# Optimization experiments

Measured on AMD Instinct MI355X. Metric: run time of the kernel, lower is better.

## Reference

```python
import jax, jax.numpy as jnp
import numpy as np

B, D, H, W, C = 2, 6, 64, 64, 192
NH = 8                      # num heads
HD = C // NH                # head dim
E, K, HID = 8, 2, 384       # experts, top_k, d_hidden
WS = (2, 8, 8)              # window size (Wd, Wh, Ww)
SS = (1, 4, 4)              # shift size
N = WS[0] * WS[1] * WS[2]   # 128 tokens per window
NW = (D // WS[0]) * (H // WS[1]) * (W // WS[2])  # 192 windows per sample
SCALE = HD ** -0.5


def _rel_pos_index():
    coords = np.stack(np.meshgrid(np.arange(WS[0]), np.arange(WS[1]), np.arange(WS[2]), indexing='ij'))
    coords = coords.reshape(3, -1)
    rel = (coords[:, :, None] - coords[:, None, :]).transpose(1, 2, 0).astype(np.int64)
    rel[..., 0] += WS[0] - 1
    rel[..., 1] += WS[1] - 1
    rel[..., 2] += WS[2] - 1
    rel[..., 0] *= (2 * WS[1] - 1) * (2 * WS[2] - 1)
    rel[..., 1] *= (2 * WS[2] - 1)
    return rel.sum(-1)  # (N, N)


def _sine_pos_encoding():
    # VRT get_sine_position_encoding(window_size[1:], dim//2, normalize=True)
    h, w, nf = WS[1], WS[2], C // 2
    scale = 2 * np.pi
    y = np.cumsum(np.ones((1, h, w)), 1)
    x = np.cumsum(np.ones((1, h, w)), 2)
    y = y / (y[:, -1:, :] + 1e-6) * scale
    x = x / (x[:, :, -1:] + 1e-6) * scale
    dim_t = 10000.0 ** (2 * (np.arange(nf) // 2) / nf)
    px = x[..., None] / dim_t
    py = y[..., None] / dim_t
    px = np.stack([np.sin(px[..., 0::2]), np.cos(px[..., 1::2])], -1).reshape(1, h, w, -1)
    py = np.stack([np.sin(py[..., 0::2]), np.cos(py[..., 1::2])], -1).reshape(1, h, w, -1)
    return np.concatenate([py, px], -1).reshape(1, h * w, C).astype(np.float32)


def _compute_mask():
    # VRT compute_mask for cyclic shift
    img = np.zeros((1, D, H, W, 1))
    cnt = 0
    for d in (slice(0, -WS[0]), slice(-WS[0], -SS[0]), slice(-SS[0], None)):
        for h in (slice(0, -WS[1]), slice(-WS[1], -SS[1]), slice(-SS[1], None)):
            for w in (slice(0, -WS[2]), slice(-WS[2], -SS[2]), slice(-SS[2], None)):
                img[:, d, h, w, :] = cnt
                cnt += 1
    mw = img.reshape(1, D // WS[0], WS[0], H // WS[1], WS[1], W // WS[2], WS[2], 1)
    mw = mw.transpose(0, 1, 3, 5, 2, 4, 6, 7).reshape(-1, N)
    am = mw[:, None, :] - mw[:, :, None]
    return np.where(am != 0, -100.0, 0.0).astype(np.float32)  # (NW, N, N)


RP_INDEX = jnp.asarray(_rel_pos_index())
POS_BIAS = jnp.asarray(_sine_pos_encoding())  # (1, Wh*Ww, C)


def layernorm(x, w, b):
    mu = x.mean(-1, keepdims=True)
    var = ((x - mu) ** 2).mean(-1, keepdims=True)
    return (x - mu) * jax.lax.rsqrt(var + 1e-5) * w + b


def window_partition(x):
    x = x.reshape(B, D // WS[0], WS[0], H // WS[1], WS[1], W // WS[2], WS[2], C)
    return x.transpose(0, 1, 3, 5, 2, 4, 6, 7).reshape(-1, N, C)


def window_reverse(wx):
    x = wx.reshape(B, D // WS[0], H // WS[1], W // WS[2], WS[0], WS[1], WS[2], C)
    return x.transpose(0, 1, 4, 2, 5, 3, 6, 7).reshape(B, D, H, W, C)


def _attn(q, k, v, mask, bias):
    # q,k,v: (B_, NH, n, HD); mask: (NW, N, N) or None; bias: (NH, n, n) or None
    n = q.shape[2]
    a = jnp.einsum('bhnd,bhmd->bhnm', q * SCALE, k)
    if bias is not None:
        a = a + bias[None]
    if mask is not None:
        a = a.reshape(-1, NW, NH, n, n) + mask[None, :, None, :n, :n]
        a = a.reshape(-1, NH, n, n)
    a = jax.nn.softmax(a, -1)
    o = jnp.einsum('bhnm,bhmd->bhnd', a, v)
    return o.transpose(0, 2, 1, 3).reshape(o.shape[0], n, NH * HD)


def reference(x, mask_matrix, n1_w, n1_b, qkv_self_w, qkv_self_b, qkv_mut_w, qkv_mut_b,
              rpb_table, proj_w, proj_b, n2_w, n2_b, gate_w, gate_b, W1, b1, W2, b2):
    # ---- part 1: shifted 3D window attention (self + mutual) ----
    xn = layernorm(x, n1_w, n1_b)
    xs = jnp.roll(xn, shift=(-SS[0], -SS[1], -SS[2]), axis=(1, 2, 3))
    xw = window_partition(xs)  # (B_, N, C)
    B_ = xw.shape[0]

    def qkv_split(t):
        t = t.reshape(B_, -1, 3, NH, HD).transpose(2, 0, 3, 1, 4)
        return t[0], t[1], t[2]

    # self attention with relative position bias
    q, k, v = qkv_split(xw @ qkv_self_w + qkv_self_b)
    bias = rpb_table[RP_INDEX.reshape(-1)].reshape(N, N, NH).transpose(2, 0, 1)
    x_self = _attn(q, k, v, mask_matrix, bias)

    # mutual attention between the two frames of each window
    xm = xw + jnp.tile(POS_BIAS, (1, 2, 1))
    q, k, v = qkv_split(xm @ qkv_mut_w + qkv_mut_b)
    half = N // 2
    q1, q2 = q[:, :, :half], q[:, :, half:]
    k1, k2 = k[:, :, :half], k[:, :, half:]
    v1, v2 = v[:, :, :half], v[:, :, half:]
    x1 = _attn(q2, k1, v1, mask_matrix, None)
    x2 = _attn(q1, k2, v2, mask_matrix, None)
    x_out = jnp.concatenate([jnp.concatenate([x1, x2], 1), x_self], 2)  # (B_, N, 2C)

    attn_out = x_out @ proj_w + proj_b  # (B_, N, C)
    xr = window_reverse(attn_out)
    xr = jnp.roll(xr, shift=SS, axis=(1, 2, 3))
    x = x + xr

    # ---- part 2: MoE FFN (top-2 gate, per-expert 2-layer MLP, weighted combine) ----
    xn = layernorm(x, n2_w, n2_b).reshape(-1, C)  # (T, C)
    logits = xn @ gate_w + gate_b  # (T, E)
    top_val, top_idx = jax.lax.top_k(logits, K)
    scores = jax.nn.softmax(top_val, -1)  # (T, K)
    cw = (jax.nn.one_hot(top_idx, E, dtype=xn.dtype) * scores[..., None]).sum(1)  # (T, E)

    def body(acc, p):
        w1, bb1, w2, bb2, cwe = p
        hdd = jax.nn.gelu(xn @ w1 + bb1, approximate=False)
        return acc + cwe[:, None] * (hdd @ w2 + bb2), None

    moe_out, _ = jax.lax.scan(body, jnp.zeros_like(xn), (W1, b1, W2, b2, cw.T))
    return x + moe_out.reshape(B, D, H, W, C)


def setup_inputs() -> dict:
    key = jax.random.key(0)
    ks = jax.random.split(key, 8)
    s = 0.02
    tbl = (2 * WS[0] - 1) * (2 * WS[1] - 1) * (2 * WS[2] - 1)
    return dict(
        x=jax.random.normal(ks[0], (B, D, H, W, C), jnp.float32),
        mask_matrix=jnp.asarray(_compute_mask()),
        n1_w=jnp.ones((C,), jnp.float32), n1_b=jnp.zeros((C,), jnp.float32),
        qkv_self_w=jax.random.normal(ks[1], (C, 3 * C), jnp.float32) * s,
        qkv_self_b=jnp.zeros((3 * C,), jnp.float32),
        qkv_mut_w=jax.random.normal(ks[2], (C, 3 * C), jnp.float32) * s,
        qkv_mut_b=jnp.zeros((3 * C,), jnp.float32),
        rpb_table=jax.random.normal(ks[3], (tbl, NH), jnp.float32) * s,
        proj_w=jax.random.normal(ks[4], (2 * C, C), jnp.float32) * s,
        proj_b=jnp.zeros((C,), jnp.float32),
        n2_w=jnp.ones((C,), jnp.float32), n2_b=jnp.zeros((C,), jnp.float32),
        gate_w=jax.random.normal(ks[5], (C, E), jnp.float32) * s,
        gate_b=jnp.zeros((E,), jnp.float32),
        W1=jax.random.normal(ks[6], (E, C, HID), jnp.float32) * s,
        b1=jnp.zeros((E, HID), jnp.float32),
        W2=jax.random.normal(ks[7], (E, HID, C), jnp.float32) * s,
        b2=jnp.zeros((E, C), jnp.float32),
    )
```

## Files before the change

kernel.cpp:

```cpp
#include <hip/hip_runtime.h>
#include <hip/hip_bf16.h>

#define NW_ 192
#define NWIN 384
#define NTOK 128
#define CC 192
#define NHD 8
#define HD 24
#define QKVC 576
#define NROWS 49152
#define HIDN 384
#define SCALE_Q 0.20412414523193154f

typedef __hip_bfloat16 bf16;
typedef __attribute__((ext_vector_type(8))) short s16x8;
typedef __attribute__((ext_vector_type(4))) float f32x4;

__device__ __forceinline__ float waveRedSum(float v) {
    v += __shfl_xor(v, 32);
    v += __shfl_xor(v, 16);
    v += __shfl_xor(v, 8);
    v += __shfl_xor(v, 4);
    v += __shfl_xor(v, 2);
    v += __shfl_xor(v, 1);
    return v;
}

__device__ __forceinline__ size_t row_to_x(int r) {
    int wb = r >> 7;
    int n = r & 127;
    int b = wb / NW_;
    int rem = wb % NW_;
    int wd = rem >> 6;
    int wh = (rem >> 3) & 7;
    int ww = rem & 7;
    int id = n >> 6;
    int ih = (n >> 3) & 7;
    int iw = n & 7;
    int d = (wd * 2 + id + 1) % 6;
    int h = (wh * 8 + ih + 4) & 63;
    int w = (ww * 8 + iw + 4) & 63;
    return ((size_t)((b * 6 + d) * 64 + h) * 64 + w) * CC;
}

__device__ __forceinline__ void split_store(float v, bf16* hi, bf16* lo) {
    bf16 h = __float2bfloat16(v);
    *hi = h;
    *lo = __float2bfloat16(v - __bfloat162float(h));
}

__global__ void zero_counts(int* counts) {
    if (threadIdx.x < 8) counts[threadIdx.x] = 0;
}

__global__ __launch_bounds__(256) void transpose_w(
    const float* __restrict__ in, bf16* __restrict__ out_hi,
    bf16* __restrict__ out_lo, int K, int N) {
    size_t total = (size_t)K * N;
    in += (size_t)blockIdx.z * total;
    out_hi += (size_t)blockIdx.z * total;
    int t = blockIdx.x * 256 + threadIdx.x;
    if (t >= (int)total) return;
    int n = t / K, k = t % K;
    float v = in[(size_t)k * N + n];
    bf16 h = __float2bfloat16(v);
    out_hi[t] = h;
    if (out_lo) {
        out_lo += (size_t)blockIdx.z * total;
        out_lo[t] = __float2bfloat16(v - __bfloat162float(h));
    }
}

__global__ __launch_bounds__(256) void build_rpbx(
    const float* __restrict__ rpb, float* __restrict__ rpbx) {
    int idx = blockIdx.x * 256 + threadIdx.x;
    int q = idx >> 7, k = idx & 127;
    int dn = q >> 6, hn = (q >> 3) & 7, wn = q & 7;
    int dm = k >> 6, hm = (k >> 3) & 7, wm = k & 7;
    int ridx = (dn - dm + 1) * 225 + (hn - hm + 7) * 15 + (wn - wm + 7);
#pragma unroll
    for (int h = 0; h < 8; ++h)
        rpbx[h * 16384 + idx] = rpb[ridx * 8 + h];
}

__global__ __launch_bounds__(256) void ln1_partition(
    const float* __restrict__ x, const float* __restrict__ n1w,
    const float* __restrict__ n1b, bf16* __restrict__ xw_hi,
    bf16* __restrict__ xw_lo) {
    int r = blockIdx.x * 4 + (threadIdx.x >> 6);
    int t = threadIdx.x & 63;
    const float* src = x + row_to_x(r);
    float v0 = src[t], v1 = src[t + 64], v2 = src[t + 128];
    float mu = waveRedSum(v0 + v1 + v2) * (1.0f / 192.0f);
    float d0 = v0 - mu, d1 = v1 - mu, d2 = v2 - mu;
    float var = waveRedSum(d0 * d0 + d1 * d1 + d2 * d2) * (1.0f / 192.0f);
    float rstd = rsqrtf(var + 1e-5f);
    size_t b = (size_t)r * CC;
    split_store(d0 * rstd * n1w[t]       + n1b[t],       xw_hi + b + t,       xw_lo + b + t);
    split_store(d1 * rstd * n1w[t + 64]  + n1b[t + 64],  xw_hi + b + t + 64,  xw_lo + b + t + 64);
    split_store(d2 * rstd * n1w[t + 128] + n1b[t + 128], xw_hi + b + t + 128, xw_lo + b + t + 128);
}

__global__ __launch_bounds__(256) void add_posbias(
    bf16* __restrict__ hi, bf16* __restrict__ lo) {
    int idx = blockIdx.x * 256 + threadIdx.x;
    if (idx >= NROWS * CC) return;
    int c = idx % CC;
    int r = idx / CC;
    int n = r & 127;
    int tkn = n & 63;
    int h = tkn >> 3, w = tkn & 7;
    const float twopi_over = 6.283185307179586f / (8.0f + 1e-6f);
    float coord = (c < 96) ? (h + 1) * twopi_over : (w + 1) * twopi_over;
    int cc = (c < 96) ? c : c - 96;
    int j = cc >> 1;
    float v = coord * __expf(-0.1918820910968785f * (float)j);
    float pe = (cc & 1) ? __cosf(v) : __sinf(v);
    float val = __bfloat162float(hi[idx]) + __bfloat162float(lo[idx]) + pe;
    split_store(val, hi + idx, lo + idx);
}

template <int EPI, int GSHIFT, bool GATHER, bool SPLIT>
__global__ __launch_bounds__(256) void mgemm(
    const bf16* __restrict__ A, const bf16* __restrict__ Alo, int ldA,
    const bf16* __restrict__ Wt, const bf16* __restrict__ Wtlo, int wStrideE,
    const float* __restrict__ bias, int biasStrideE,
    float* __restrict__ Cf, bf16* __restrict__ Cb,
    int M, int K, int N,
    const int* __restrict__ counts, const int* __restrict__ lists,
    const float* __restrict__ wts, const float* __restrict__ xres) {
    int e = blockIdx.z;
    int Mq = counts ? counts[e] : M;
    int bm = blockIdx.x * 128;
    if (bm >= Mq) return;
    int bn = blockIdx.y * 64;
    const int lbase = e * NROWS;
    __shared__ __align__(16) bf16 As[128][72];
    __shared__ __align__(16) bf16 Bs[64][72];
    __shared__ __align__(16) bf16 Asl[(SPLIT ? 128 : 1)][72];
    __shared__ __align__(16) bf16 Bsl[(SPLIT ? 64 : 1)][72];
    int t = threadIdx.x;
    int arow = t >> 1, acol = (t & 1) * 32;
    int brow = t >> 2, bcol = (t & 3) * 16;
    size_t aoff;
    if (GATHER) {
        int p = bm + arow;
        int a = lists[lbase + (p < Mq ? p : 0)];
        aoff = (size_t)(a >> GSHIFT) * (size_t)ldA + acol;
    } else {
        aoff = (size_t)(bm + arow) * (size_t)ldA + acol;
    }
    size_t boff = (size_t)e * wStrideE + (size_t)(bn + brow) * K + bcol;
    int wv = t >> 6, l = t & 63;
    int wvm = wv >> 1, wvn = wv & 1;
    int fr = l & 15, fg = l >> 4;
    f32x4 acc[4][2];
#pragma unroll
    for (int mf = 0; mf < 4; ++mf)
#pragma unroll
        for (int nf = 0; nf < 2; ++nf) acc[mf][nf] = (f32x4){0.f, 0.f, 0.f, 0.f};
    for (int k0 = 0; k0 < K; k0 += 64) {
        __syncthreads();
#pragma unroll
        for (int u = 0; u < 4; ++u)
            *(int4*)&As[arow][acol + u * 8] = *(const int4*)(A + aoff + k0 + u * 8);
        *(int4*)&Bs[brow][bcol]     = *(const int4*)(Wt + boff + k0);
        *(int4*)&Bs[brow][bcol + 8] = *(const int4*)(Wt + boff + k0 + 8);
        if (SPLIT) {
#pragma unroll
            for (int u = 0; u < 4; ++u)
                *(int4*)&Asl[arow][acol + u * 8] = *(const int4*)(Alo + aoff + k0 + u * 8);
            *(int4*)&Bsl[brow][bcol]     = *(const int4*)(Wtlo + boff + k0);
            *(int4*)&Bsl[brow][bcol + 8] = *(const int4*)(Wtlo + boff + k0 + 8);
        }
        __syncthreads();
#pragma unroll
        for (int ks = 0; ks < 2; ++ks) {
            s16x8 ah[4], al[4], bh[2], bl[2];
#pragma unroll
            for (int mf = 0; mf < 4; ++mf) {
                ah[mf] = *(const s16x8*)&As[wvm * 64 + mf * 16 + fr][ks * 32 + fg * 8];
                if (SPLIT) al[mf] = *(const s16x8*)&Asl[wvm * 64 + mf * 16 + fr][ks * 32 + fg * 8];
            }
#pragma unroll
            for (int nf = 0; nf < 2; ++nf) {
                bh[nf] = *(const s16x8*)&Bs[wvn * 32 + nf * 16 + fr][ks * 32 + fg * 8];
                if (SPLIT) bl[nf] = *(const s16x8*)&Bsl[wvn * 32 + nf * 16 + fr][ks * 32 + fg * 8];
            }
#pragma unroll
            for (int mf = 0; mf < 4; ++mf)
#pragma unroll
                for (int nf = 0; nf < 2; ++nf) {
                    acc[mf][nf] = __builtin_amdgcn_mfma_f32_16x16x32_bf16(ah[mf], bh[nf], acc[mf][nf], 0, 0, 0);
                    if (SPLIT) {
                        acc[mf][nf] = __builtin_amdgcn_mfma_f32_16x16x32_bf16(ah[mf], bl[nf], acc[mf][nf], 0, 0, 0);
                        acc[mf][nf] = __builtin_amdgcn_mfma_f32_16x16x32_bf16(al[mf], bh[nf], acc[mf][nf], 0, 0, 0);
                    }
                }
        }
    }
#pragma unroll
    for (int mf = 0; mf < 4; ++mf) {
        int row0 = bm + wvm * 64 + mf * 16 + fg * 4;
        if (EPI == 0) {
#pragma unroll
            for (int nf = 0; nf < 2; ++nf) {
                int c = bn + wvn * 32 + nf * 16 + fr;
                float bv = bias[c];
#pragma unroll
                for (int i = 0; i < 4; ++i)
                    Cf[(size_t)(row0 + i) * N + c] = acc[mf][nf][i] + bv;
            }
        } else if (EPI == 1) {
            size_t sr[4];
#pragma unroll
            for (int i = 0; i < 4; ++i) sr[i] = row_to_x(row0 + i);
#pragma unroll
            for (int nf = 0; nf < 2; ++nf) {
                int c = bn + wvn * 32 + nf * 16 + fr;
                float bv = bias[c];
#pragma unroll
                for (int i = 0; i < 4; ++i)
                    Cf[sr[i] + c] = xres[sr[i] + c] + acc[mf][nf][i] + bv;
            }
        } else if (EPI == 2) {
            const float* bp = bias + (size_t)e * biasStrideE;
#pragma unroll
            for (int i = 0; i < 4; ++i) {
                int p = row0 + i;
                if (p < Mq) {
                    int a = lists[lbase + p];
#pragma unroll
                    for (int nf = 0; nf < 2; ++nf) {
                        int c = bn + wvn * 32 + nf * 16 + fr;
                        float v = acc[mf][nf][i] + bp[c];
                        float g = 0.5f * v * (1.0f + erff(v * 0.7071067811865476f));
                        Cb[(size_t)a * HIDN + c] = __float2bfloat16(g);
                    }
                }
            }
        } else if (EPI == 3) {
            const float* bp = bias + (size_t)e * biasStrideE;
#pragma unroll
            for (int i = 0; i < 4; ++i) {
                int p = row0 + i;
                if (p < Mq) {
                    int a = lists[lbase + p];
                    int r = a >> 1;
                    float w = wts[lbase + p];
#pragma unroll
                    for (int nf = 0; nf < 2; ++nf) {
                        int c = bn + wvn * 32 + nf * 16 + fr;
                        atomicAdd(&Cf[(size_t)r * CC + c], w * (acc[mf][nf][i] + bp[c]));
                    }
                }
            }
        } else {
            const size_t S0 = (size_t)NROWS * 192;
            const size_t S1 = (size_t)NROWS * 24;
#pragma unroll
            for (int nf = 0; nf < 2; ++nf) {
                int c = bn + wvn * 32 + nf * 16 + fr;
                int which = c / 192;
                int rem = c - which * 192;
                int hh = rem / 24;
                int d = rem - hh * 24;
                float bv = bias[c];
                bf16* hb = Cb + (size_t)(2 * which) * S0 + (size_t)hh * S1;
                bf16* lb = Cb + (size_t)(2 * which + 1) * S0 + (size_t)hh * S1;
#pragma unroll
                for (int i = 0; i < 4; ++i) {
                    float v = acc[mf][nf][i] + bv;
                    if (which == 0) v *= SCALE_Q;
                    size_t o = (size_t)(row0 + i) * 24 + d;
                    split_store(v, hb + o, lb + o);
                }
            }
        }
    }
}

template <bool SELF>
__global__ __launch_bounds__(256) void attn_mfma(
    const bf16* __restrict__ qkvp, const float* __restrict__ mask,
    const float* __restrict__ rpbx, bf16* __restrict__ cat_hi,
    bf16* __restrict__ cat_lo) {
    constexpr int NT = SELF ? 128 : 64;
    constexpr int KT = NT / 16;
    constexpr int CPW = NT / 64;
    constexpr int KS = NT / 32;
    const size_t S0 = (size_t)NROWS * 192;
    const size_t S1 = (size_t)NROWS * 24;

    int wb = blockIdx.x, hh = blockIdx.y;
    int hf = SELF ? 0 : blockIdx.z;
    int qbase = wb * NTOK + (SELF ? 0 : (hf ? 0 : 64));
    int kvbase = wb * NTOK + (SELF ? 0 : (hf ? 64 : 0));
    int t = threadIdx.x;
    int wv = t >> 6, l = t & 63, fr = l & 15, fg = l >> 4;

    __shared__ __align__(16) ushort Vth[32][144];
    __shared__ __align__(16) ushort Vtl[32][144];
    __shared__ float linv_s[NT];

    {
        constexpr int PPT = 256 / NT;
        constexpr int DP = 24 / PPT;
        int tok = t % NT;
        int part = t / NT;
        const ushort* vh = (const ushort*)(qkvp + 4 * S0) + hh * S1 +
                           (size_t)(kvbase + tok) * 24 + part * DP;
        const ushort* vl = (const ushort*)(qkvp + 5 * S0) + hh * S1 +
                           (size_t)(kvbase + tok) * 24 + part * DP;
#pragma unroll
        for (int u = 0; u < DP; ++u) {
            Vth[part * DP + u][tok] = vh[u];
            Vtl[part * DP + u][tok] = vl[u];
        }
    }

    s16x8 zf = {0, 0, 0, 0, 0, 0, 0, 0};
    f32x4 st[KT][CPW];
#pragma unroll
    for (int kt = 0; kt < KT; ++kt)
#pragma unroll
        for (int c = 0; c < CPW; ++c) st[kt][c] = (f32x4){0.f, 0.f, 0.f, 0.f};

    s16x8 qfh[CPW], qfl[CPW];
#pragma unroll
    for (int c = 0; c < CPW; ++c) {
        int qt = wv * CPW + c;
        const bf16* qrow = qkvp + hh * S1 + (size_t)(qbase + qt * 16 + fr) * 24 + fg * 8;
        qfh[c] = (fg < 3) ? *(const s16x8*)qrow : zf;
        qfl[c] = (fg < 3) ? *(const s16x8*)(qrow + S0) : zf;
    }
#pragma unroll
    for (int kt = 0; kt < KT; ++kt) {
        const bf16* krow = qkvp + 2 * S0 + hh * S1 + (size_t)(kvbase + kt * 16 + fr) * 24 + fg * 8;
        s16x8 kh = (fg < 3) ? *(const s16x8*)krow : zf;
        s16x8 kl = (fg < 3) ? *(const s16x8*)(krow + S0) : zf;
#pragma unroll
        for (int c = 0; c < CPW; ++c) {
            st[kt][c] = __builtin_amdgcn_mfma_f32_16x16x32_bf16(kh, qfh[c], st[kt][c], 0, 0, 0);
            st[kt][c] = __builtin_amdgcn_mfma_f32_16x16x32_bf16(kh, qfl[c], st[kt][c], 0, 0, 0);
            st[kt][c] = __builtin_amdgcn_mfma_f32_16x16x32_bf16(kl, qfh[c], st[kt][c], 0, 0, 0);
        }
    }

    uint phq[KT][CPW][2], plq[KT][CPW][2];
#pragma unroll
    for (int c = 0; c < CPW; ++c) {
        int q = (wv * CPW + c) * 16 + fr;
        const float* mrow = mask + ((size_t)(wb % NW_) * NTOK + q) * NTOK;
        const float* brow = rpbx + ((size_t)hh * NTOK + q) * NTOK;
        float mx = -1e30f;
#pragma unroll
        for (int kt = 0; kt < KT; ++kt) {
            int k0 = kt * 16 + fg * 4;
            float4 mk = *(const float4*)(mrow + k0);
            if (SELF) {
                float4 bs = *(const float4*)(brow + k0);
                mk.x += bs.x; mk.y += bs.y; mk.z += bs.z; mk.w += bs.w;
            }
            st[kt][c][0] += mk.x; st[kt][c][1] += mk.y;
            st[kt][c][2] += mk.z; st[kt][c][3] += mk.w;
#pragma unroll
            for (int i = 0; i < 4; ++i) mx = fmaxf(mx, st[kt][c][i]);
        }
        mx = fmaxf(mx, __shfl_xor(mx, 16));
        mx = fmaxf(mx, __shfl_xor(mx, 32));
        float ls = 0.f;
#pragma unroll
        for (int kt = 0; kt < KT; ++kt)
#pragma unroll
            for (int i = 0; i < 4; ++i) {
                float pv = __expf(st[kt][c][i] - mx);
                st[kt][c][i] = pv;
                ls += pv;
            }
        ls += __shfl_xor(ls, 16);
        ls += __shfl_xor(ls, 32);
        if (fg == 0) linv_s[q] = 1.0f / ls;
#pragma unroll
        for (int kt = 0; kt < KT; ++kt) {
            ushort hb[4], lb[4];
#pragma unroll
            for (int i = 0; i < 4; ++i) {
                float pv = st[kt][c][i];
                bf16 ph = __float2bfloat16(pv);
                hb[i] = *(ushort*)&ph;
                bf16 pl = __float2bfloat16(pv - __bfloat162float(ph));
                lb[i] = *(ushort*)&pl;
            }
            phq[kt][c][0] = (uint)hb[0] | ((uint)hb[1] << 16);
            phq[kt][c][1] = (uint)hb[2] | ((uint)hb[3] << 16);
            plq[kt][c][0] = (uint)lb[0] | ((uint)lb[1] << 16);
            plq[kt][c][1] = (uint)lb[2] | ((uint)lb[3] << 16);
        }
    }
    __syncthreads();

    f32x4 oacc[CPW][2];
#pragma unroll
    for (int rt = 0; rt < CPW; ++rt)
#pragma unroll
        for (int ct = 0; ct < 2; ++ct) oacc[rt][ct] = (f32x4){0.f, 0.f, 0.f, 0.f};

    int sA = fr + 32 * (fg & 1);
    int sB = sA + 16;
    bool tsel = fg >= 2;
#pragma unroll
    for (int ks = 0; ks < KS; ++ks) {
        s16x8 bh[2], bl[2];
#pragma unroll
        for (int ct = 0; ct < 2; ++ct) {
            bh[ct] = *(const s16x8*)&Vth[ct * 16 + fr][ks * 32 + fg * 8];
            bl[ct] = *(const s16x8*)&Vtl[ct * 16 + fr][ks * 32 + fg * 8];
        }
#pragma unroll
        for (int rt = 0; rt < CPW; ++rt) {
            union { uint u[4]; s16x8 v; } ah, al;
            uint x0, x1;
            x0 = __shfl(phq[2 * ks][rt][0], sA); x1 = __shfl(phq[2 * ks + 1][rt][0], sA);
            ah.u[0] = tsel ? x1 : x0;
            x0 = __shfl(phq[2 * ks][rt][1], sA); x1 = __shfl(phq[2 * ks + 1][rt][1], sA);
            ah.u[1] = tsel ? x1 : x0;
            x0 = __shfl(phq[2 * ks][rt][0], sB); x1 = __shfl(phq[2 * ks + 1][rt][0], sB);
            ah.u[2] = tsel ? x1 : x0;
            x0 = __shfl(phq[2 * ks][rt][1], sB); x1 = __shfl(phq[2 * ks + 1][rt][1], sB);
            ah.u[3] = tsel ? x1 : x0;
            x0 = __shfl(plq[2 * ks][rt][0], sA); x1 = __shfl(plq[2 * ks + 1][rt][0], sA);
            al.u[0] = tsel ? x1 : x0;
            x0 = __shfl(plq[2 * ks][rt][1], sA); x1 = __shfl(plq[2 * ks + 1][rt][1], sA);
            al.u[1] = tsel ? x1 : x0;
            x0 = __shfl(plq[2 * ks][rt][0], sB); x1 = __shfl(plq[2 * ks + 1][rt][0], sB);
            al.u[2] = tsel ? x1 : x0;
            x0 = __shfl(plq[2 * ks][rt][1], sB); x1 = __shfl(plq[2 * ks + 1][rt][1], sB);
            al.u[3] = tsel ? x1 : x0;
#pragma unroll
            for (int ct = 0; ct < 2; ++ct) {
                oacc[rt][ct] = __builtin_amdgcn_mfma_f32_16x16x32_bf16(ah.v, bh[ct], oacc[rt][ct], 0, 0, 0);
                oacc[rt][ct] = __builtin_amdgcn_mfma_f32_16x16x32_bf16(ah.v, bl[ct], oacc[rt][ct], 0, 0, 0);
                oacc[rt][ct] = __builtin_amdgcn_mfma_f32_16x16x32_bf16(al.v, bh[ct], oacc[rt][ct], 0, 0, 0);
            }
        }
    }

#pragma unroll
    for (int rt = 0; rt < CPW; ++rt)
#pragma unroll
        for (int ct = 0; ct < 2; ++ct) {
            int d = ct * 16 + fr;
            if (d < 24) {
#pragma unroll
                for (int i = 0; i < 4; ++i) {
                    int q = (wv * CPW + rt) * 16 + fg * 4 + i;
                    float val = oacc[rt][ct][i] * linv_s[q];
                    int otok = SELF ? q : (hf ? 64 + q : q);
                    size_t ob = (size_t)(wb * NTOK + otok) * 384 + (SELF ? 192 : 0) + hh * 24 + d;
                    split_store(val, cat_hi + ob, cat_lo + ob);
                }
            }
        }
}

__global__ __launch_bounds__(256) void ln2_gate(
    const float* __restrict__ xin, const float* __restrict__ n2w,
    const float* __restrict__ n2b, const float* __restrict__ gw,
    const float* __restrict__ gb, bf16* __restrict__ xn2,
    uchar2* __restrict__ ee, float2* __restrict__ ww) {
    __shared__ float sh[4][192];
    int wave = threadIdx.x >> 6;
    int t = threadIdx.x & 63;
    int r = blockIdx.x * 4 + wave;
    const float* src = xin + (size_t)r * CC;
    float v0 = src[t], v1 = src[t + 64], v2 = src[t + 128];
    float mu = waveRedSum(v0 + v1 + v2) * (1.0f / 192.0f);
    float d0 = v0 - mu, d1 = v1 - mu, d2 = v2 - mu;
    float var = waveRedSum(d0 * d0 + d1 * d1 + d2 * d2) * (1.0f / 192.0f);
    float rstd = rsqrtf(var + 1e-5f);
    float o0 = d0 * rstd * n2w[t] + n2b[t];
    float o1 = d1 * rstd * n2w[t + 64] + n2b[t + 64];
    float o2 = d2 * rstd * n2w[t + 128] + n2b[t + 128];
    bf16* dst = xn2 + (size_t)r * CC;
    dst[t] = __float2bfloat16(o0);
    dst[t + 64] = __float2bfloat16(o1);
    dst[t + 128] = __float2bfloat16(o2);
    sh[wave][t] = o0; sh[wave][t + 64] = o1; sh[wave][t + 128] = o2;
    __builtin_amdgcn_wave_barrier();
    int e = t & 7, ch = t >> 3;
    float part = 0.0f;
    for (int c = ch * 24; c < ch * 24 + 24; ++c) part += sh[wave][c] * gw[c * 8 + e];
    part += __shfl_xor(part, 8);
    part += __shfl_xor(part, 16);
    part += __shfl_xor(part, 32);
    float logit = part + gb[e];
    float b1v = -1e30f, b2v = -1e30f;
    int i1 = 0, i2 = 0;
    for (int qe = 0; qe < 8; ++qe) {
        float lv = __shfl(logit, qe);
        if (lv > b1v) { b2v = b1v; i2 = i1; b1v = lv; i1 = qe; }
        else if (lv > b2v) { b2v = lv; i2 = qe; }
    }
    if (t == 0) {
        float e2 = __expf(b2v - b1v);
        float inv = 1.0f / (1.0f + e2);
        ee[r] = make_uchar2((unsigned char)i1, (unsigned char)i2);
        ww[r] = make_float2(inv, e2 * inv);
    }
}

__global__ __launch_bounds__(256) void route(
    const uchar2* __restrict__ ee, const float2* __restrict__ ww,
    int* __restrict__ counts, int* __restrict__ lists, float* __restrict__ wts) {
    __shared__ int lcnt[8];
    __shared__ int lbase[8];
    int t = threadIdx.x;
    int r = blockIdx.x * 256 + t;
    if (t < 8) lcnt[t] = 0;
    __syncthreads();
    uchar2 e = ee[r];
    float2 w = ww[r];
    int p1 = atomicAdd(&lcnt[e.x], 1);
    int p2 = atomicAdd(&lcnt[e.y], 1);
    __syncthreads();
    if (t < 8) lbase[t] = atomicAdd(&counts[t], lcnt[t]);
    __syncthreads();
    int d1 = e.x * NROWS + lbase[e.x] + p1;
    int d2 = e.y * NROWS + lbase[e.y] + p2;
    lists[d1] = r * 2;
    wts[d1] = w.x;
    lists[d2] = r * 2 + 1;
    wts[d2] = w.y;
}

extern "C" void kernel_launch(void* const* d_in, const int* in_sizes, int n_in,
                              void* d_out, int out_size, void* d_ws, size_t ws_size,
                              hipStream_t stream) {
    const float* x     = (const float*)d_in[0];
    const float* mask  = (const float*)d_in[1];
    const float* n1w   = (const float*)d_in[2];
    const float* n1b   = (const float*)d_in[3];
    const float* qkvsw = (const float*)d_in[4];
    const float* qkvsb = (const float*)d_in[5];
    const float* qkvmw = (const float*)d_in[6];
    const float* qkvmb = (const float*)d_in[7];
    const float* rpb   = (const float*)d_in[8];
    const float* projw = (const float*)d_in[9];
    const float* projb = (const float*)d_in[10];
    const float* n2w   = (const float*)d_in[11];
    const float* n2b   = (const float*)d_in[12];
    const float* gw    = (const float*)d_in[13];
    const float* gb    = (const float*)d_in[14];
    const float* W1    = (const float*)d_in[15];
    const float* b1    = (const float*)d_in[16];
    const float* W2    = (const float*)d_in[17];
    const float* b2    = (const float*)d_in[18];
    float* out = (float*)d_out;
    const size_t S0 = (size_t)NROWS * 192;

    char* p = (char*)d_ws;
    bf16* xw_hi = (bf16*)p;     p += S0 * 2;
    bf16* xw_lo = (bf16*)p;     p += S0 * 2;
    bf16* qkvp = (bf16*)p;
    bf16* H = (bf16*)p;         p += S0 * 6 * 2;
    bf16* cat_hi = (bf16*)p;    p += (size_t)NROWS * 384 * 2;
    bf16* cat_lo = (bf16*)p;    p += (size_t)NROWS * 384 * 2;
    bf16* xn2 = (bf16*)p;       p += S0 * 2;
    int* counts = (int*)p;      p += 32;
    int* lists = (int*)p;       p += (size_t)8 * NROWS * 4;
    float* wts = (float*)p;     p += (size_t)8 * NROWS * 4;
    uchar2* ee = (uchar2*)p;    p += (size_t)NROWS * 2;
    float2* ww = (float2*)p;    p += (size_t)NROWS * 8;
    float* rpbx = (float*)p;    p += (size_t)8 * 16384 * 4;
    bf16* qkvswT_hi = (bf16*)p; p += 110592 * 2;
    bf16* qkvswT_lo = (bf16*)p; p += 110592 * 2;
    bf16* qkvmwT_hi = (bf16*)p; p += 110592 * 2;
    bf16* qkvmwT_lo = (bf16*)p; p += 110592 * 2;
    bf16* projwT_hi = (bf16*)p; p += 73728 * 2;
    bf16* projwT_lo = (bf16*)p; p += 73728 * 2;
    bf16* W1T = (bf16*)p;       p += (size_t)8 * 73728 * 2;
    bf16* W2T = (bf16*)p;       p += (size_t)8 * 73728 * 2;

    zero_counts<<<1, 64, 0, stream>>>(counts);
    build_rpbx<<<64, 256, 0, stream>>>(rpb, rpbx);
    transpose_w<<<dim3(432, 1, 1), 256, 0, stream>>>(qkvsw, qkvswT_hi, qkvswT_lo, 192, 576);
    transpose_w<<<dim3(432, 1, 1), 256, 0, stream>>>(qkvmw, qkvmwT_hi, qkvmwT_lo, 192, 576);
    transpose_w<<<dim3(288, 1, 1), 256, 0, stream>>>(projw, projwT_hi, projwT_lo, 384, 192);
    transpose_w<<<dim3(288, 1, 8), 256, 0, stream>>>(W1, W1T, nullptr, 192, 384);
    transpose_w<<<dim3(288, 1, 8), 256, 0, stream>>>(W2, W2T, nullptr, 384, 192);

    ln1_partition<<<NROWS / 4, 256, 0, stream>>>(x, n1w, n1b, xw_hi, xw_lo);
    mgemm<4, 0, false, true><<<dim3(384, 9, 1), 256, 0, stream>>>(
        xw_hi, xw_lo, CC, qkvswT_hi, qkvswT_lo, 0, qkvsb, 0, nullptr, qkvp,
        NROWS, CC, QKVC, nullptr, nullptr, nullptr, nullptr);
    attn_mfma<true><<<dim3(NWIN, NHD), 256, 0, stream>>>(qkvp, mask, rpbx, cat_hi, cat_lo);
    add_posbias<<<(NROWS * CC) / 256, 256, 0, stream>>>(xw_hi, xw_lo);
    mgemm<4, 0, false, true><<<dim3(384, 9, 1), 256, 0, stream>>>(
        xw_hi, xw_lo, CC, qkvmwT_hi, qkvmwT_lo, 0, qkvmb, 0, nullptr, qkvp,
        NROWS, CC, QKVC, nullptr, nullptr, nullptr, nullptr);
    attn_mfma<false><<<dim3(NWIN, NHD, 2), 256, 0, stream>>>(qkvp, mask, rpbx, cat_hi, cat_lo);
    mgemm<1, 0, false, true><<<dim3(384, 3, 1), 256, 0, stream>>>(
        cat_hi, cat_lo, 384, projwT_hi, projwT_lo, 0, projb, 0, out, nullptr,
        NROWS, 384, CC, nullptr, nullptr, nullptr, x);
    ln2_gate<<<NROWS / 4, 256, 0, stream>>>(out, n2w, n2b, gw, gb, xn2, ee, ww);
    route<<<NROWS / 256, 256, 0, stream>>>(ee, ww, counts, lists, wts);
    mgemm<2, 1, true, false><<<dim3(384, 6, 8), 256, 0, stream>>>(
        xn2, nullptr, CC, W1T, nullptr, 73728, b1, HIDN, nullptr, H,
        NROWS, CC, HIDN, counts, lists, nullptr, nullptr);
    mgemm<3, 0, true, false><<<dim3(384, 3, 8), 256, 0, stream>>>(
        H, nullptr, HIDN, W2T, nullptr, 73728, b2, CC, out, nullptr,
        NROWS, HIDN, CC, counts, lists, wts, nullptr);
}
```

Baseline: 701.4 us.

## Load GEMM tiles directly to LDS with XOR-swizzled layout; fold count reset

Replaces register-staged global-to-shared copies in the mgemm kernel with global_load_lds direct-to-LDS 16-byte loads, using an unpadded 128-byte row layout with an XOR swizzle to avoid bank conflicts on MFMA fragment reads. This removes VGPR staging and the padded layout. It also drops the separate zero_counts launch by having block 0 of ln2_gate reset the expert counters. Correctness depends on the per-lane address mapping matching the wave-wide LDS write pattern of the builtin.

```diff
diff --git a/kernel.cpp b/kernel.cpp
--- a/kernel.cpp
+++ b/kernel.cpp
@@ -15,6 +15,13 @@
 typedef __hip_bfloat16 bf16;
 typedef __attribute__((ext_vector_type(8))) short s16x8;
 typedef __attribute__((ext_vector_type(4))) float f32x4;
+
+typedef __attribute__((address_space(3))) unsigned as3u;
+typedef const __attribute__((address_space(1))) unsigned as1u;
+
+__device__ __forceinline__ void gl16(const void* g, void* l) {
+    __builtin_amdgcn_global_load_lds((as1u*)g, (as3u*)l, 16, 0, 0);
+}
 
 __device__ __forceinline__ float waveRedSum(float v) {
     v += __shfl_xor(v, 32);
@@ -47,10 +54,6 @@
     bf16 h = __float2bfloat16(v);
     *hi = h;
     *lo = __float2bfloat16(v - __bfloat162float(h));
-}
-
-__global__ void zero_counts(int* counts) {
-    if (threadIdx.x < 8) counts[threadIdx.x] = 0;
 }
 
 __global__ __launch_bounds__(256) void transpose_w(
@@ -135,57 +138,70 @@
     if (bm >= Mq) return;
     int bn = blockIdx.y * 64;
     const int lbase = e * NROWS;
-    __shared__ __align__(16) bf16 As[128][72];
-    __shared__ __align__(16) bf16 Bs[64][72];
-    __shared__ __align__(16) bf16 Asl[(SPLIT ? 128 : 1)][72];
-    __shared__ __align__(16) bf16 Bsl[(SPLIT ? 64 : 1)][72];
+    __shared__ __align__(16) char Ah[128 * 128];
+    __shared__ __align__(16) char Bh[64 * 128];
+    __shared__ __align__(16) char Al[SPLIT ? 128 * 128 : 16];
+    __shared__ __align__(16) char Bl[SPLIT ? 64 * 128 : 16];
     int t = threadIdx.x;
-    int arow = t >> 1, acol = (t & 1) * 32;
-    int brow = t >> 2, bcol = (t & 3) * 16;
-    size_t aoff;
-    if (GATHER) {
-        int p = bm + arow;
-        int a = lists[lbase + (p < Mq ? p : 0)];
-        aoff = (size_t)(a >> GSHIFT) * (size_t)ldA + acol;
-    } else {
-        aoff = (size_t)(bm + arow) * (size_t)ldA + acol;
-    }
-    size_t boff = (size_t)e * wStrideE + (size_t)(bn + brow) * K + bcol;
     int wv = t >> 6, l = t & 63;
+    int lrow = l >> 3;
+    int lperm = ((l & 7) ^ lrow) * 8;
     int wvm = wv >> 1, wvn = wv & 1;
     int fr = l & 15, fg = l >> 4;
+
+    size_t aOff[4];
+#pragma unroll
+    for (int u = 0; u < 4; ++u) {
+        int j = wv * 4 + u;
+        int p = bm + j * 8 + lrow;
+        int row;
+        if (GATHER) {
+            int a = lists[lbase + (p < Mq ? p : 0)];
+            row = a >> GSHIFT;
+        } else row = p;
+        aOff[u] = (size_t)row * (size_t)ldA + lperm;
+    }
+    size_t bOff[2];
+#pragma unroll
+    for (int u = 0; u < 2; ++u) {
+        int j = wv * 2 + u;
+        bOff[u] = (size_t)e * wStrideE + (size_t)(bn + j * 8 + lrow) * K + lperm;
+    }
+
     f32x4 acc[4][2];
 #pragma unroll
     for (int mf = 0; mf < 4; ++mf)
 #pragma unroll
         for (int nf = 0; nf < 2; ++nf) acc[mf][nf] = (f32x4){0.f, 0.f, 0.f, 0.f};
+
     for (int k0 = 0; k0 < K; k0 += 64) {
         __syncthreads();
 #pragma unroll
-        for (int u = 0; u < 4; ++u)
-            *(int4*)&As[arow][acol + u * 8] = *(const int4*)(A + aoff + k0 + u * 8);
-        *(int4*)&Bs[brow][bcol]     = *(const int4*)(Wt + boff + k0);
-        *(int4*)&Bs[brow][bcol + 8] = *(const int4*)(Wt + boff + k0 + 8);
-        if (SPLIT) {
-#pragma unroll
-            for (int u = 0; u < 4; ++u)
-                *(int4*)&Asl[arow][acol + u * 8] = *(const int4*)(Alo + aoff + k0 + u * 8);
-            *(int4*)&Bsl[brow][bcol]     = *(const int4*)(Wtlo + boff + k0);
-            *(int4*)&Bsl[brow][bcol + 8] = *(const int4*)(Wtlo + boff + k0 + 8);
+        for (int u = 0; u < 4; ++u) {
+            gl16(A + aOff[u] + k0, Ah + (wv * 4 + u) * 1024);
+            if (SPLIT) gl16(Alo + aOff[u] + k0, Al + (wv * 4 + u) * 1024);
+        }
+#pragma unroll
+        for (int u = 0; u < 2; ++u) {
+            gl16(Wt + bOff[u] + k0, Bh + (wv * 2 + u) * 1024);
+            if (SPLIT) gl16(Wtlo + bOff[u] + k0, Bl + (wv * 2 + u) * 1024);
         }
         __syncthreads();
 #pragma unroll
         for (int ks = 0; ks < 2; ++ks) {
+            int kx = ((ks * 4 + fg) ^ (fr & 7)) << 4;
             s16x8 ah[4], al[4], bh[2], bl[2];
 #pragma unroll
             for (int mf = 0; mf < 4; ++mf) {
-                ah[mf] = *(const s16x8*)&As[wvm * 64 + mf * 16 + fr][ks * 32 + fg * 8];
-                if (SPLIT) al[mf] = *(const s16x8*)&Asl[wvm * 64 + mf * 16 + fr][ks * 32 + fg * 8];
+                int rb = (wvm * 64 + mf * 16 + fr) * 128;
+                ah[mf] = *(const s16x8*)(Ah + rb + kx);
+                if (SPLIT) al[mf] = *(const s16x8*)(Al + rb + kx);
             }
 #pragma unroll
             for (int nf = 0; nf < 2; ++nf) {
-                bh[nf] = *(const s16x8*)&Bs[wvn * 32 + nf * 16 + fr][ks * 32 + fg * 8];
-                if (SPLIT) bl[nf] = *(const s16x8*)&Bsl[wvn * 32 + nf * 16 + fr][ks * 32 + fg * 8];
+                int rb = (wvn * 32 + nf * 16 + fr) * 128;
+                bh[nf] = *(const s16x8*)(Bh + rb + kx);
+                if (SPLIT) bl[nf] = *(const s16x8*)(Bl + rb + kx);
             }
 #pragma unroll
             for (int mf = 0; mf < 4; ++mf)
@@ -468,7 +484,8 @@
     const float* __restrict__ xin, const float* __restrict__ n2w,
     const float* __restrict__ n2b, const float* __restrict__ gw,
     const float* __restrict__ gb, bf16* __restrict__ xn2,
-    uchar2* __restrict__ ee, float2* __restrict__ ww) {
+    uchar2* __restrict__ ee, float2* __restrict__ ww, int* __restrict__ counts) {
+    if (blockIdx.x == 0 && threadIdx.x < 8) counts[threadIdx.x] = 0;
     __shared__ float sh[4][192];
     int wave = threadIdx.x >> 6;
     int t = threadIdx.x & 63;
@@ -582,7 +599,6 @@
     bf16* W1T = (bf16*)p;       p += (size_t)8 * 73728 * 2;
     bf16* W2T = (bf16*)p;       p += (size_t)8 * 73728 * 2;
 
-    zero_counts<<<1, 64, 0, stream>>>(counts);
     build_rpbx<<<64, 256, 0, stream>>>(rpb, rpbx);
     transpose_w<<<dim3(432, 1, 1), 256, 0, stream>>>(qkvsw, qkvswT_hi, qkvswT_lo, 192, 576);
     transpose_w<<<dim3(432, 1, 1), 256, 0, stream>>>(qkvmw, qkvmwT_hi, qkvmwT_lo, 192, 576);
@@ -603,7 +619,7 @@
     mgemm<1, 0, false, true><<<dim3(384, 3, 1), 256, 0, stream>>>(
         cat_hi, cat_lo, 384, projwT_hi, projwT_lo, 0, projb, 0, out, nullptr,
         NROWS, 384, CC, nullptr, nullptr, nullptr, x);
-    ln2_gate<<<NROWS / 4, 256, 0, stream>>>(out, n2w, n2b, gw, gb, xn2, ee, ww);
+    ln2_gate<<<NROWS / 4, 256, 0, stream>>>(out, n2w, n2b, gw, gb, xn2, ee, ww, counts);
     route<<<NROWS / 256, 256, 0, stream>>>(ee, ww, counts, lists, wts);
     mgemm<2, 1, true, false><<<dim3(384, 6, 8), 256, 0, stream>>>(
         xn2, nullptr, CC, W1T, nullptr, 73728, b1, HIDN, nullptr, H,
```

Result: faster. 678.7 us (-3.2%).
